# Performance work log

Measured on AMD Instinct MI355X. Metric: run time of the kernel, lower is better.

## Reference

```python
import jax, jax.numpy as jnp
import numpy as np
import math

D_MODEL = 1024
NUM_HEADS = 16
HEAD_DIM = D_MODEL // NUM_HEADS
GAMMA = 1.0
B, T = 2, 2048
PHI_F = 8


def setup_inputs() -> dict:
    key = jax.random.key(0)
    ks = jax.random.split(key, 16)
    s = 0.02
    return {
        "query": jax.random.normal(ks[0], (B, T, D_MODEL), jnp.float32),
        "key": jax.random.normal(ks[1], (B, T, D_MODEL), jnp.float32),
        "value": jax.random.normal(ks[2], (B, T, D_MODEL), jnp.float32),
        "phi": jax.random.uniform(ks[3], (B, T, PHI_F), jnp.float32),
        "logvar": jax.random.normal(ks[4], (B, T, PHI_F), jnp.float32),
        "Wq": jax.random.normal(ks[5], (D_MODEL, D_MODEL), jnp.float32) * s,
        "bq": jnp.zeros((D_MODEL,), jnp.float32),
        "Wk": jax.random.normal(ks[6], (D_MODEL, D_MODEL), jnp.float32) * s,
        "bk": jnp.zeros((D_MODEL,), jnp.float32),
        "Wv": jax.random.normal(ks[7], (D_MODEL, D_MODEL), jnp.float32) * s,
        "bv": jnp.zeros((D_MODEL,), jnp.float32),
        "Wo": jax.random.normal(ks[8], (D_MODEL, D_MODEL), jnp.float32) * s,
        "bo": jnp.zeros((D_MODEL,), jnp.float32),
        "w_sigma": jnp.float32(1.0),
        "w_phi": jnp.float32(1.0),
    }


def reference(query, key, value, phi, logvar, Wq, bq, Wk, bk, Wv, bv, Wo, bo, w_sigma, w_phi):
    Bsz, Tq, _ = query.shape
    # projections (torch Linear: x @ W.T + b), split into heads -> (B, H, T, hd)
    def proj(x, W, b):
        return (x @ W.T + b).reshape(Bsz, Tq, NUM_HEADS, HEAD_DIM).transpose(0, 2, 1, 3)
    q = proj(query, Wq, bq)
    k = proj(key, Wk, bk)
    v = proj(value, Wv, bv)
    # raw scores (B, H, Tq, Tk)
    scores = jnp.einsum("bhqd,bhkd->bhqk", q, k) / math.sqrt(HEAD_DIM)
    # per-query token scalar biases: mean over feature dim -> (B, 1, T, 1)
    lv = logvar.mean(axis=-1)[:, None, :, None]
    ph = phi.mean(axis=-1)[:, None, :, None]
    scores = scores - w_sigma * lv
    scores = (scores - w_phi * (1.0 - ph)) / jnp.maximum(ph ** GAMMA, 1e-6)
    attn = jax.nn.softmax(scores, axis=-1)
    out = jnp.einsum("bhqk,bhkd->bhqd", attn, v)
    out = out.transpose(0, 2, 1, 3).reshape(Bsz, Tq, D_MODEL)
    return out @ Wo.T + bo
```

## Files before the change

kernel.cpp:

```cpp
#include <hip/hip_runtime.h>


typedef __bf16 bf16x8 __attribute__((ext_vector_type(8)));
typedef __bf16 bf16x4 __attribute__((ext_vector_type(4)));
typedef float f32x4 __attribute__((ext_vector_type(4)));
typedef unsigned short u16;
typedef unsigned int u32;
typedef u16 u16x8 __attribute__((ext_vector_type(8)));

#define GLD_TO_LDS(g, l) __builtin_amdgcn_global_load_lds( \
    (const __attribute__((address_space(1))) void*)(g),    \
    (__attribute__((address_space(3))) void*)(l), 16, 0, 0)

__device__ __forceinline__ u16 f2b(float f) {
  u32 u = __builtin_bit_cast(u32, f);
  u += 0x7fffu + ((u >> 16) & 1u);
  return (u16)(u >> 16);
}

__global__ __launch_bounds__(256) void prep_kernel(
    const float* __restrict__ query, const float* __restrict__ key,
    const float* __restrict__ value, const float* __restrict__ Wq,
    const float* __restrict__ Wk, const float* __restrict__ Wv,
    const float* __restrict__ Wo, const float* __restrict__ phi,
    u16* __restrict__ Xq, u16* __restrict__ Xk, u16* __restrict__ Xv,
    u16* __restrict__ Wqb, u16* __restrict__ Wkb, u16* __restrict__ Wvb,
    u16* __restrict__ Wob, float* __restrict__ rscale)
{
  const long gid = (long)blockIdx.x * 256 + threadIdx.x;
  const long e = gid * 4;
  const float* src; u16* dst; long off;
  if (e < 4194304L)       { src = query; dst = Xq;  off = e; }
  else if (e < 8388608L)  { src = key;   dst = Xk;  off = e - 4194304L; }
  else if (e < 12582912L) { src = value; dst = Xv;  off = e - 8388608L; }
  else if (e < 13631488L) { src = Wq;    dst = Wqb; off = e - 12582912L; }
  else if (e < 14680064L) { src = Wk;    dst = Wkb; off = e - 13631488L; }
  else if (e < 15728640L) { src = Wv;    dst = Wvb; off = e - 14680064L; }
  else                    { src = Wo;    dst = Wob; off = e - 15728640L; }
  const float4 v = *(const float4*)(src + off);
  ushort4 o;
  o.x = f2b(v.x); o.y = f2b(v.y); o.z = f2b(v.z); o.w = f2b(v.w);
  *(ushort4*)(dst + off) = o;

  if (gid < 4096) {
    const float4 p0 = *(const float4*)(phi + gid * 8);
    const float4 p1 = *(const float4*)(phi + gid * 8 + 4);
    const float mean = (p0.x + p0.y + p0.z + p0.w + p1.x + p1.y + p1.z + p1.w) * 0.125f;
    rscale[gid] = 1.4426950408889634f / (8.0f * fmaxf(mean, 1e-6f));
  }
}

template<int MODE>
__device__ __forceinline__ void gemm_body(
    u16 (*As)[4096], u16 (*Bs)[4096], int m0, int n0,
    const u16* __restrict__ A, const u16* __restrict__ Bw,
    const float* __restrict__ bias, void* __restrict__ Cout)
{
  constexpr int K = 1024;
  const int t = threadIdx.x;
  const int lane = t & 63, w = t >> 6;
  const int g = lane >> 4, c = lane & 15;
  const int srow = t >> 2, skc = (t & 3) * 8;
  const u16* gA = A + (size_t)(m0 + srow) * K + skc;
  const u16* gB = Bw + (size_t)(n0 + srow) * K + skc;
  const int wm = (w >> 1) * 64, wn = (w & 1) * 64;

  f32x4 acc[4][4] = {};

#define STG(b_, k0_) do {                              \
    GLD_TO_LDS(gA + (k0_), &As[b_][w * 512]);          \
    GLD_TO_LDS(gA + 64 * K + (k0_), &As[b_][w * 512 + 2048]); \
    GLD_TO_LDS(gB + (k0_), &Bs[b_][w * 512]);          \
    GLD_TO_LDS(gB + 64 * K + (k0_), &Bs[b_][w * 512 + 2048]); \
  } while (0)

  STG(0, 0);
  for (int i = 0; i < 32; ++i) {
    const int buf = i & 1;
    if (i < 31) {
      STG(buf ^ 1, (i + 1) * 32);
      asm volatile("s_waitcnt vmcnt(4)" ::: "memory");
    } else {
      asm volatile("s_waitcnt vmcnt(0)" ::: "memory");
    }
    __builtin_amdgcn_s_barrier();
    bf16x8 af[4], bfr[4];
#pragma unroll
    for (int mi = 0; mi < 4; ++mi)
      af[mi] = *(const bf16x8*)(&As[buf][0] + (wm + mi * 16 + c) * 32 + g * 8);
#pragma unroll
    for (int ni = 0; ni < 4; ++ni)
      bfr[ni] = *(const bf16x8*)(&Bs[buf][0] + (wn + ni * 16 + c) * 32 + g * 8);
#pragma unroll
    for (int mi = 0; mi < 4; ++mi)
#pragma unroll
      for (int ni = 0; ni < 4; ++ni)
        acc[mi][ni] = __builtin_amdgcn_mfma_f32_16x16x32_bf16(
            af[mi], bfr[ni], acc[mi][ni], 0, 0, 0);
    __builtin_amdgcn_s_barrier();
  }
#undef STG

#pragma unroll
  for (int ni = 0; ni < 4; ++ni) {
    const int ncol = n0 + wn + ni * 16 + c;
    const float bv = bias[ncol];
#pragma unroll
    for (int mi = 0; mi < 4; ++mi) {
#pragma unroll
      for (int r = 0; r < 4; ++r) {
        const int mrow = m0 + wm + mi * 16 + g * 4 + r;
        const float val = acc[mi][ni][r] + bv;
        if (MODE == 0) {
          const int bb = mrow >> 11, tt = mrow & 2047;
          const int hh = ncol >> 6, dd = ncol & 63;
          ((u16*)Cout)[((((size_t)bb * 16 + hh) * 2048 + tt) << 6) + dd] = f2b(val);
        } else {
          ((float*)Cout)[(size_t)mrow * 1024 + ncol] = val;
        }
      }
    }
  }
}

__global__ __launch_bounds__(256) void gemm_qkv_kernel(
    const u16* __restrict__ Xq, const u16* __restrict__ Xk, const u16* __restrict__ Xv,
    const u16* __restrict__ Wqb, const u16* __restrict__ Wkb, const u16* __restrict__ Wvb,
    const float* __restrict__ bq, const float* __restrict__ bk, const float* __restrict__ bv,
    u16* __restrict__ Qh, u16* __restrict__ Kh, u16* __restrict__ Vh)
{
  __shared__ __align__(16) u16 As[2][4096], Bs[2][4096];
  const u32 n = blockIdx.z * 256u + blockIdx.y * 8u + blockIdx.x;
  const u32 nl = (n & 7u) * 96u + (n >> 3);
  const int bx = nl & 7, by = (nl >> 3) & 31, bz = nl >> 8;
  const u16* A = (bz == 0) ? Xq : (bz == 1) ? Xk : Xv;
  const u16* W = (bz == 0) ? Wqb : (bz == 1) ? Wkb : Wvb;
  const float* bias = (bz == 0) ? bq : (bz == 1) ? bk : bv;
  u16* C = (bz == 0) ? Qh : (bz == 1) ? Kh : Vh;
  gemm_body<0>(As, Bs, by * 128, bx * 128, A, W, bias, C);
}

__global__ __launch_bounds__(256) void gemm_o_kernel(
    const u16* __restrict__ Oh, const u16* __restrict__ Wob,
    const float* __restrict__ bo, float* __restrict__ out)
{
  __shared__ __align__(16) u16 As[2][4096], Bs[2][4096];
  const u32 n = blockIdx.y * 8u + blockIdx.x;
  const u32 nl = (n & 7u) * 32u + (n >> 3);
  gemm_body<1>(As, Bs, (int)(nl >> 3) * 128, (int)(nl & 7) * 128, Oh, Wob, bo, out);
}

__global__ __launch_bounds__(256) void transpose_v_kernel(
    const u16* __restrict__ Vh, u16* __restrict__ Vt)
{
  __shared__ __align__(16) u16 tile[64][72];
  const int bh = blockIdx.y, t0 = blockIdx.x * 64;
  const int tid = threadIdx.x;
  const int r = tid >> 3, cc = (tid & 7) * 8;
  const u16* src = Vh + ((size_t)bh * 2048 + t0) * 64;
#pragma unroll
  for (int it = 0; it < 2; ++it)
    *(u16x8*)&tile[r + 32 * it][cc] = *(const u16x8*)(src + (size_t)(r + 32 * it) * 64 + cc);
  __syncthreads();
  u16* dst = Vt + (size_t)bh * 64 * 2048 + t0;
#pragma unroll
  for (int it = 0; it < 2; ++it) {
    const int d = r + 32 * it;
    u16x8 v;
#pragma unroll
    for (int j = 0; j < 8; ++j) v[j] = tile[cc + j][d];
    *(u16x8*)(dst + (size_t)d * 2048 + cc) = v;
  }
}

__global__ __launch_bounds__(256) void attn_kernel(
    const u16* __restrict__ Qh, const u16* __restrict__ Kh,
    const u16* __restrict__ Vt, const float* __restrict__ rscale,
    u16* __restrict__ Oh)
{
  __shared__ __align__(16) u16 Ks[2][4096];
  __shared__ __align__(16) u16 Vs[2][4096];

  const u32 orig = blockIdx.y * 32 + blockIdx.x;
  const u32 newL = (orig & 7u) * 128u + (orig >> 3);
  const int qx = newL & 31, bh = newL >> 5;
  const int b = bh >> 4, h = bh & 15;

  const int t = threadIdx.x;
  const int w = t >> 6, lane = t & 63;
  const int g = lane >> 4, c = lane & 15;
  const int q0 = qx * 64 + w * 16;
  const int swz = (c & 7) << 4;

  const u16* Qb = Qh + (size_t)bh * (2048 * 64);
  const u16* Kb = Kh + (size_t)bh * (2048 * 64);
  const u16* Vb = Vt + (size_t)bh * (64 * 2048);

  const int sr = t >> 3;
  const int sx = ((t & 7) ^ (sr & 7)) * 8;

  const float rs = rscale[b * 2048 + q0 + c];
  bf16x8 qf0, qf1;
  {
    const u16x8 a0 = *(const u16x8*)(Qb + (size_t)(q0 + c) * 64 + g * 8);
    const u16x8 a1 = *(const u16x8*)(Qb + (size_t)(q0 + c) * 64 + 32 + g * 8);
    u16x8 o0, o1;
#pragma unroll
    for (int j = 0; j < 8; ++j) {
      o0[j] = f2b(__builtin_bit_cast(float, (u32)a0[j] << 16) * rs);
      o1[j] = f2b(__builtin_bit_cast(float, (u32)a1[j] << 16) * rs);
    }
    qf0 = __builtin_bit_cast(bf16x8, o0);
    qf1 = __builtin_bit_cast(bf16x8, o1);
  }

  float m = -3.0e38f, l = 0.0f;
  f32x4 acc[4] = {};

#define STAGE(buf_, kc_) do {                                         \
    const u16* kg0 = Kb + (size_t)((kc_) + sr) * 64 + sx;             \
    const u16* kg1 = Kb + (size_t)((kc_) + 32 + sr) * 64 + sx;        \
    const u16* vg0 = Vb + (size_t)sr * 2048 + (kc_) + sx;             \
    const u16* vg1 = Vb + (size_t)(32 + sr) * 2048 + (kc_) + sx;      \
    u16* kd = &Ks[buf_][w * 512];                                     \
    u16* vd = &Vs[buf_][w * 512];                                     \
    GLD_TO_LDS(kg0, kd);                                              \
    GLD_TO_LDS(kg1, kd + 2048);                                       \
    GLD_TO_LDS(vg0, vd);                                              \
    GLD_TO_LDS(vg1, vd + 2048);                                       \
  } while (0)

  STAGE(0, 0);

  for (int kc = 0; kc < 2048; kc += 64) {
    const int buf = (kc >> 6) & 1;
    if (kc + 64 < 2048) {
      STAGE(buf ^ 1, kc + 64);
      asm volatile("s_waitcnt vmcnt(4)" ::: "memory");
    } else {
      asm volatile("s_waitcnt vmcnt(0)" ::: "memory");
    }
    __builtin_amdgcn_s_barrier();

    const u16* Kt = &Ks[buf][0];
    const u16* Vq = &Vs[buf][0];

    f32x4 s[4];
#pragma unroll
    for (int j = 0; j < 4; ++j) {
      const int rk = j * 16 + c;
      const bf16x8 k0 = *(const bf16x8*)(Kt + rk * 64 + ((((g << 4)) ^ swz) >> 1));
      const bf16x8 k1 = *(const bf16x8*)(Kt + rk * 64 + (((64 | (g << 4)) ^ swz) >> 1));
      const f32x4 z = {};
      s[j] = __builtin_amdgcn_mfma_f32_16x16x32_bf16(k0, qf0, z, 0, 0, 0);
      s[j] = __builtin_amdgcn_mfma_f32_16x16x32_bf16(k1, qf1, s[j], 0, 0, 0);
    }

    float tl = s[0][0];
#pragma unroll
    for (int j = 0; j < 4; ++j)
#pragma unroll
      for (int r = 0; r < 4; ++r) tl = fmaxf(tl, s[j][r]);
    if (__any(tl > m + 8.0f)) {
      tl = fmaxf(tl, __shfl_xor(tl, 16));
      tl = fmaxf(tl, __shfl_xor(tl, 32));
      const float mn = fmaxf(m, tl);
      const float corr = __builtin_amdgcn_exp2f(m - mn);
      m = mn;
      l *= corr;
#pragma unroll
      for (int dt = 0; dt < 4; ++dt)
#pragma unroll
        for (int r = 0; r < 4; ++r) acc[dt][r] *= corr;
    }

    float p[4][4];
#pragma unroll
    for (int j = 0; j < 4; ++j)
#pragma unroll
      for (int r = 0; r < 4; ++r) {
        p[j][r] = __builtin_amdgcn_exp2f(s[j][r] - m);
        l += p[j][r];
      }
    bf16x8 pb0, pb1;
#pragma unroll
    for (int jj = 0; jj < 8; ++jj) {
      pb0[jj] = (__bf16)p[jj >> 2][jj & 3];
      pb1[jj] = (__bf16)p[2 + (jj >> 2)][jj & 3];
    }

#pragma unroll
    for (int dt = 0; dt < 4; ++dt) {
      const int rv = dt * 16 + c;
      const u16* vrow = Vq + rv * 64;
      const int xr = (rv & 7) << 4;
      bf16x8 va0, va1;
      const bf16x4 a0 = *(const bf16x4*)(vrow + (((g * 8) ^ xr) >> 1));
      const bf16x4 a1 = *(const bf16x4*)(vrow + (((32 + g * 8) ^ xr) >> 1));
      const bf16x4 a2 = *(const bf16x4*)(vrow + (((64 + g * 8) ^ xr) >> 1));
      const bf16x4 a3 = *(const bf16x4*)(vrow + (((96 + g * 8) ^ xr) >> 1));
#pragma unroll
      for (int j = 0; j < 4; ++j) {
        va0[j] = a0[j]; va0[4 + j] = a1[j];
        va1[j] = a2[j]; va1[4 + j] = a3[j];
      }
      acc[dt] = __builtin_amdgcn_mfma_f32_16x16x32_bf16(va0, pb0, acc[dt], 0, 0, 0);
      acc[dt] = __builtin_amdgcn_mfma_f32_16x16x32_bf16(va1, pb1, acc[dt], 0, 0, 0);
    }

    __builtin_amdgcn_s_barrier();
  }
#undef STAGE

  l += __shfl_xor(l, 16);
  l += __shfl_xor(l, 32);
  const float inv = 1.0f / l;

#pragma unroll
  for (int dt = 0; dt < 4; ++dt)
#pragma unroll
    for (int r = 0; r < 4; ++r) {
      const int trow = q0 + c;
      const int dd = dt * 16 + g * 4 + r;
      Oh[(((size_t)b * 2048 + trow) * 16 + h) * 64 + dd] = f2b(acc[dt][r] * inv);
    }
}

extern "C" void kernel_launch(void* const* d_in, const int* in_sizes, int n_in,
                              void* d_out, int out_size, void* d_ws, size_t ws_size,
                              hipStream_t stream) {
  const float* query = (const float*)d_in[0];
  const float* key_  = (const float*)d_in[1];
  const float* value = (const float*)d_in[2];
  const float* phi   = (const float*)d_in[3];
  const float* Wq = (const float*)d_in[5];
  const float* bq = (const float*)d_in[6];
  const float* Wk = (const float*)d_in[7];
  const float* bk = (const float*)d_in[8];
  const float* Wv = (const float*)d_in[9];
  const float* bv = (const float*)d_in[10];
  const float* Wo = (const float*)d_in[11];
  const float* bo = (const float*)d_in[12];

  char* ws = (char*)d_ws;
  const size_t MB = 1u << 20;
  u16* Xq  = (u16*)(ws);
  u16* Xk  = (u16*)(ws + 8 * MB);
  u16* Xv  = (u16*)(ws + 16 * MB);
  u16* Wqb = (u16*)(ws + 24 * MB);
  u16* Wkb = (u16*)(ws + 26 * MB);
  u16* Wvb = (u16*)(ws + 28 * MB);
  u16* Wob = (u16*)(ws + 30 * MB);
  u16* Qh  = (u16*)(ws + 32 * MB);
  u16* Kh  = (u16*)(ws + 40 * MB);
  u16* Vh  = (u16*)(ws + 48 * MB);
  float* rscale = (float*)(ws + 56 * MB);
  u16* Oh = Xq;
  u16* Vt = Xk;

  prep_kernel<<<16384, 256, 0, stream>>>(query, key_, value, Wq, Wk, Wv, Wo, phi,
                                         Xq, Xk, Xv, Wqb, Wkb, Wvb, Wob, rscale);
  gemm_qkv_kernel<<<dim3(8, 32, 3), 256, 0, stream>>>(Xq, Xk, Xv, Wqb, Wkb, Wvb,
                                                      bq, bk, bv, Qh, Kh, Vh);
  transpose_v_kernel<<<dim3(32, 32), 256, 0, stream>>>(Vh, Vt);
  attn_kernel<<<dim3(32, 32), 256, 0, stream>>>(Qh, Kh, Vt, rscale, Oh);
  gemm_o_kernel<<<dim3(8, 32), 256, 0, stream>>>(Oh, Wob, bo, (float*)d_out);
}
```

Baseline: 258.4 us.

## Fuse V transpose into QKV GEMM epilogue, shuffle P operand, add MFMA priority

The V projection epilogue now writes the transposed (d-major) layout directly, which removes the separate transpose kernel and its round trip through global memory. In the attention kernel, V fragments are read as full 16-byte swizzled LDS loads, and the P operand is redistributed across lanes with shuffles so that its layout matches. s_setprio is raised around MFMA clusters in both the GEMM and attention loops. The costs are strided 2-byte scattered stores in the V epilogue, extra cross-lane shuffles per iteration, and a dependence on the new lane mapping being correct.

```diff
diff --git a/kernel.cpp b/kernel.cpp
--- a/kernel.cpp
+++ b/kernel.cpp
@@ -2,11 +2,12 @@
 
 
 typedef __bf16 bf16x8 __attribute__((ext_vector_type(8)));
-typedef __bf16 bf16x4 __attribute__((ext_vector_type(4)));
+typedef __bf16 bf16x2 __attribute__((ext_vector_type(2)));
 typedef float f32x4 __attribute__((ext_vector_type(4)));
 typedef unsigned short u16;
 typedef unsigned int u32;
 typedef u16 u16x8 __attribute__((ext_vector_type(8)));
+typedef u32 u32x4 __attribute__((ext_vector_type(4)));
 
 #define GLD_TO_LDS(g, l) __builtin_amdgcn_global_load_lds( \
     (const __attribute__((address_space(1))) void*)(g),    \
@@ -91,12 +92,14 @@
 #pragma unroll
     for (int ni = 0; ni < 4; ++ni)
       bfr[ni] = *(const bf16x8*)(&Bs[buf][0] + (wn + ni * 16 + c) * 32 + g * 8);
+    __builtin_amdgcn_s_setprio(1);
 #pragma unroll
     for (int mi = 0; mi < 4; ++mi)
 #pragma unroll
       for (int ni = 0; ni < 4; ++ni)
         acc[mi][ni] = __builtin_amdgcn_mfma_f32_16x16x32_bf16(
             af[mi], bfr[ni], acc[mi][ni], 0, 0, 0);
+    __builtin_amdgcn_s_setprio(0);
     __builtin_amdgcn_s_barrier();
   }
 #undef STG
@@ -115,6 +118,10 @@
           const int bb = mrow >> 11, tt = mrow & 2047;
           const int hh = ncol >> 6, dd = ncol & 63;
           ((u16*)Cout)[((((size_t)bb * 16 + hh) * 2048 + tt) << 6) + dd] = f2b(val);
+        } else if (MODE == 2) {
+          const int bb = mrow >> 11, tt = mrow & 2047;
+          const int hh = ncol >> 6, dd = ncol & 63;
+          ((u16*)Cout)[((((size_t)bb * 16 + hh) * 64 + dd) << 11) + tt] = f2b(val);
         } else {
           ((float*)Cout)[(size_t)mrow * 1024 + ncol] = val;
         }
@@ -127,17 +134,19 @@
     const u16* __restrict__ Xq, const u16* __restrict__ Xk, const u16* __restrict__ Xv,
     const u16* __restrict__ Wqb, const u16* __restrict__ Wkb, const u16* __restrict__ Wvb,
     const float* __restrict__ bq, const float* __restrict__ bk, const float* __restrict__ bv,
-    u16* __restrict__ Qh, u16* __restrict__ Kh, u16* __restrict__ Vh)
+    u16* __restrict__ Qh, u16* __restrict__ Kh, u16* __restrict__ Vt)
 {
   __shared__ __align__(16) u16 As[2][4096], Bs[2][4096];
   const u32 n = blockIdx.z * 256u + blockIdx.y * 8u + blockIdx.x;
   const u32 nl = (n & 7u) * 96u + (n >> 3);
   const int bx = nl & 7, by = (nl >> 3) & 31, bz = nl >> 8;
-  const u16* A = (bz == 0) ? Xq : (bz == 1) ? Xk : Xv;
-  const u16* W = (bz == 0) ? Wqb : (bz == 1) ? Wkb : Wvb;
-  const float* bias = (bz == 0) ? bq : (bz == 1) ? bk : bv;
-  u16* C = (bz == 0) ? Qh : (bz == 1) ? Kh : Vh;
-  gemm_body<0>(As, Bs, by * 128, bx * 128, A, W, bias, C);
+  if (bz == 2) {
+    gemm_body<2>(As, Bs, by * 128, bx * 128, Xv, Wvb, bv, Vt);
+  } else if (bz == 1) {
+    gemm_body<0>(As, Bs, by * 128, bx * 128, Xk, Wkb, bk, Kh);
+  } else {
+    gemm_body<0>(As, Bs, by * 128, bx * 128, Xq, Wqb, bq, Qh);
+  }
 }
 
 __global__ __launch_bounds__(256) void gemm_o_kernel(
@@ -148,29 +157,6 @@
   const u32 n = blockIdx.y * 8u + blockIdx.x;
   const u32 nl = (n & 7u) * 32u + (n >> 3);
   gemm_body<1>(As, Bs, (int)(nl >> 3) * 128, (int)(nl & 7) * 128, Oh, Wob, bo, out);
-}
-
-__global__ __launch_bounds__(256) void transpose_v_kernel(
-    const u16* __restrict__ Vh, u16* __restrict__ Vt)
-{
-  __shared__ __align__(16) u16 tile[64][72];
-  const int bh = blockIdx.y, t0 = blockIdx.x * 64;
-  const int tid = threadIdx.x;
-  const int r = tid >> 3, cc = (tid & 7) * 8;
-  const u16* src = Vh + ((size_t)bh * 2048 + t0) * 64;
-#pragma unroll
-  for (int it = 0; it < 2; ++it)
-    *(u16x8*)&tile[r + 32 * it][cc] = *(const u16x8*)(src + (size_t)(r + 32 * it) * 64 + cc);
-  __syncthreads();
-  u16* dst = Vt + (size_t)bh * 64 * 2048 + t0;
-#pragma unroll
-  for (int it = 0; it < 2; ++it) {
-    const int d = r + 32 * it;
-    u16x8 v;
-#pragma unroll
-    for (int j = 0; j < 8; ++j) v[j] = tile[cc + j][d];
-    *(u16x8*)(dst + (size_t)d * 2048 + cc) = v;
-  }
 }
 
 __global__ __launch_bounds__(256) void attn_kernel(
@@ -216,6 +202,9 @@
 
   float m = -3.0e38f, l = 0.0f;
   f32x4 acc[4] = {};
+  const int src0 = ((g & 1) << 5) + c;
+  const int src1 = src0 + 16;
+  const bool hig = (g >> 1) != 0;
 
 #define STAGE(buf_, kc_) do {                                         \
     const u16* kg0 = Kb + (size_t)((kc_) + sr) * 64 + sx;             \
@@ -252,8 +241,19 @@
       const bf16x8 k0 = *(const bf16x8*)(Kt + rk * 64 + ((((g << 4)) ^ swz) >> 1));
       const bf16x8 k1 = *(const bf16x8*)(Kt + rk * 64 + (((64 | (g << 4)) ^ swz) >> 1));
       const f32x4 z = {};
+      __builtin_amdgcn_s_setprio(1);
       s[j] = __builtin_amdgcn_mfma_f32_16x16x32_bf16(k0, qf0, z, 0, 0, 0);
       s[j] = __builtin_amdgcn_mfma_f32_16x16x32_bf16(k1, qf1, s[j], 0, 0, 0);
+      __builtin_amdgcn_s_setprio(0);
+    }
+
+    bf16x8 vf[4][2];
+#pragma unroll
+    for (int dt = 0; dt < 4; ++dt) {
+      const int rv = dt * 16 + c;
+#pragma unroll
+      for (int kk = 0; kk < 2; ++kk)
+        vf[dt][kk] = *(const bf16x8*)(Vq + rv * 64 + ((((kk << 6) | (g << 4)) ^ swz) >> 1));
     }
 
     float tl = s[0][0];
@@ -282,31 +282,42 @@
         p[j][r] = __builtin_amdgcn_exp2f(s[j][r] - m);
         l += p[j][r];
       }
-    bf16x8 pb0, pb1;
-#pragma unroll
-    for (int jj = 0; jj < 8; ++jj) {
-      pb0[jj] = (__bf16)p[jj >> 2][jj & 3];
-      pb1[jj] = (__bf16)p[2 + (jj >> 2)][jj & 3];
-    }
-
+    u32 W[4][2];
+#pragma unroll
+    for (int j = 0; j < 4; ++j)
+#pragma unroll
+      for (int rp = 0; rp < 2; ++rp) {
+        bf16x2 t2;
+        t2[0] = (__bf16)p[j][2 * rp];
+        t2[1] = (__bf16)p[j][2 * rp + 1];
+        W[j][rp] = __builtin_bit_cast(u32, t2);
+      }
+    u32 R[4][2][2];
+#pragma unroll
+    for (int q = 0; q < 4; ++q)
+#pragma unroll
+      for (int rp = 0; rp < 2; ++rp) {
+        R[q][rp][0] = (u32)__shfl((int)W[q][rp], src0);
+        R[q][rp][1] = (u32)__shfl((int)W[q][rp], src1);
+      }
+    u32x4 pw0, pw1;
+#pragma unroll
+    for (int gs = 0; gs < 2; ++gs)
+#pragma unroll
+      for (int rp = 0; rp < 2; ++rp) {
+        pw0[gs * 2 + rp] = hig ? R[1][rp][gs] : R[0][rp][gs];
+        pw1[gs * 2 + rp] = hig ? R[3][rp][gs] : R[2][rp][gs];
+      }
+    const bf16x8 pb0 = __builtin_bit_cast(bf16x8, pw0);
+    const bf16x8 pb1 = __builtin_bit_cast(bf16x8, pw1);
+
+    __builtin_amdgcn_s_setprio(1);
 #pragma unroll
     for (int dt = 0; dt < 4; ++dt) {
-      const int rv = dt * 16 + c;
-      const u16* vrow = Vq + rv * 64;
-      const int xr = (rv & 7) << 4;
-      bf16x8 va0, va1;
-      const bf16x4 a0 = *(const bf16x4*)(vrow + (((g * 8) ^ xr) >> 1));
-      const bf16x4 a1 = *(const bf16x4*)(vrow + (((32 + g * 8) ^ xr) >> 1));
-      const bf16x4 a2 = *(const bf16x4*)(vrow + (((64 + g * 8) ^ xr) >> 1));
-      const bf16x4 a3 = *(const bf16x4*)(vrow + (((96 + g * 8) ^ xr) >> 1));
-#pragma unroll
-      for (int j = 0; j < 4; ++j) {
-        va0[j] = a0[j]; va0[4 + j] = a1[j];
-        va1[j] = a2[j]; va1[4 + j] = a3[j];
-      }
-      acc[dt] = __builtin_amdgcn_mfma_f32_16x16x32_bf16(va0, pb0, acc[dt], 0, 0, 0);
-      acc[dt] = __builtin_amdgcn_mfma_f32_16x16x32_bf16(va1, pb1, acc[dt], 0, 0, 0);
-    }
+      acc[dt] = __builtin_amdgcn_mfma_f32_16x16x32_bf16(vf[dt][0], pb0, acc[dt], 0, 0, 0);
+      acc[dt] = __builtin_amdgcn_mfma_f32_16x16x32_bf16(vf[dt][1], pb1, acc[dt], 0, 0, 0);
+    }
+    __builtin_amdgcn_s_setprio(0);
 
     __builtin_amdgcn_s_barrier();
   }
@@ -353,16 +364,14 @@
   u16* Wob = (u16*)(ws + 30 * MB);
   u16* Qh  = (u16*)(ws + 32 * MB);
   u16* Kh  = (u16*)(ws + 40 * MB);
-  u16* Vh  = (u16*)(ws + 48 * MB);
+  u16* Vt  = (u16*)(ws + 48 * MB);
   float* rscale = (float*)(ws + 56 * MB);
   u16* Oh = Xq;
-  u16* Vt = Xk;
 
   prep_kernel<<<16384, 256, 0, stream>>>(query, key_, value, Wq, Wk, Wv, Wo, phi,
                                          Xq, Xk, Xv, Wqb, Wkb, Wvb, Wob, rscale);
   gemm_qkv_kernel<<<dim3(8, 32, 3), 256, 0, stream>>>(Xq, Xk, Xv, Wqb, Wkb, Wvb,
-                                                      bq, bk, bv, Qh, Kh, Vh);
-  transpose_v_kernel<<<dim3(32, 32), 256, 0, stream>>>(Vh, Vt);
+                                                      bq, bk, bv, Qh, Kh, Vt);
   attn_kernel<<<dim3(32, 32), 256, 0, stream>>>(Qh, Kh, Vt, rscale, Oh);
   gemm_o_kernel<<<dim3(8, 32), 256, 0, stream>>>(Oh, Wob, bo, (float*)d_out);
 }
```

After: 296.9 us. 14.9% more time.

## Hoist V LDS reads before softmax, add setprio around MFMAs, extend V swizzle

Applied to the files above, without the earlier changes.

Moves the V fragment LDS reads ahead of the softmax so their latency overlaps the exp computations. It brackets MFMA groups with s_setprio so the scheduler favors matrix work across waves. It also adds an extra XOR bit to the V tile swizzle, matched in the transpose kernel, to reduce LDS bank conflicts. The cost is higher register pressure from holding the V fragments, and the swizzle must stay consistent between the writer and reader kernels.

```diff
diff --git a/kernel.cpp b/kernel.cpp
--- a/kernel.cpp
+++ b/kernel.cpp
@@ -163,12 +163,13 @@
     *(u16x8*)&tile[r + 32 * it][cc] = *(const u16x8*)(src + (size_t)(r + 32 * it) * 64 + cc);
   __syncthreads();
   u16* dst = Vt + (size_t)bh * 64 * 2048 + t0;
+  const int sw = (r & 8) ? 4 : 0;
 #pragma unroll
   for (int it = 0; it < 2; ++it) {
     const int d = r + 32 * it;
     u16x8 v;
 #pragma unroll
-    for (int j = 0; j < 8; ++j) v[j] = tile[cc + j][d];
+    for (int j = 0; j < 8; ++j) v[j] = tile[cc + (j ^ sw)][d];
     *(u16x8*)(dst + (size_t)d * 2048 + cc) = v;
   }
 }
@@ -252,8 +253,24 @@
       const bf16x8 k0 = *(const bf16x8*)(Kt + rk * 64 + ((((g << 4)) ^ swz) >> 1));
       const bf16x8 k1 = *(const bf16x8*)(Kt + rk * 64 + (((64 | (g << 4)) ^ swz) >> 1));
       const f32x4 z = {};
+      __builtin_amdgcn_s_setprio(1);
       s[j] = __builtin_amdgcn_mfma_f32_16x16x32_bf16(k0, qf0, z, 0, 0, 0);
       s[j] = __builtin_amdgcn_mfma_f32_16x16x32_bf16(k1, qf1, s[j], 0, 0, 0);
+      __builtin_amdgcn_s_setprio(0);
+    }
+
+    bf16x8 va[4][2];
+#pragma unroll
+    for (int dt = 0; dt < 4; ++dt) {
+      const int rv = dt * 16 + c;
+      const u16* vrow = Vq + rv * 64;
+      const int xr = ((rv & 7) << 4) | (rv & 8);
+      const bf16x4 a0 = *(const bf16x4*)(vrow + (((g * 8) ^ xr) >> 1));
+      const bf16x4 a1 = *(const bf16x4*)(vrow + (((32 + g * 8) ^ xr) >> 1));
+      const bf16x4 a2 = *(const bf16x4*)(vrow + (((64 + g * 8) ^ xr) >> 1));
+      const bf16x4 a3 = *(const bf16x4*)(vrow + (((96 + g * 8) ^ xr) >> 1));
+      va[dt][0] = __builtin_shufflevector(a0, a1, 0, 1, 2, 3, 4, 5, 6, 7);
+      va[dt][1] = __builtin_shufflevector(a2, a3, 0, 1, 2, 3, 4, 5, 6, 7);
     }
 
     float tl = s[0][0];
@@ -274,39 +291,32 @@
         for (int r = 0; r < 4; ++r) acc[dt][r] *= corr;
     }
 
-    float p[4][4];
+    f32x4 pv[4];
 #pragma unroll
     for (int j = 0; j < 4; ++j)
 #pragma unroll
-      for (int r = 0; r < 4; ++r) {
-        p[j][r] = __builtin_amdgcn_exp2f(s[j][r] - m);
-        l += p[j][r];
-      }
-    bf16x8 pb0, pb1;
-#pragma unroll
-    for (int jj = 0; jj < 8; ++jj) {
-      pb0[jj] = (__bf16)p[jj >> 2][jj & 3];
-      pb1[jj] = (__bf16)p[2 + (jj >> 2)][jj & 3];
-    }
-
+      for (int r = 0; r < 4; ++r) pv[j][r] = __builtin_amdgcn_exp2f(s[j][r] - m);
+#pragma unroll
+    for (int j = 0; j < 4; ++j)
+      l += pv[j][0] + pv[j][1] + pv[j][2] + pv[j][3];
+    bf16x4 pc[4];
+#pragma unroll
+    for (int j = 0; j < 4; ++j) {
+      pc[j][0] = (__bf16)pv[j][0];
+      pc[j][1] = (__bf16)pv[j][1];
+      pc[j][2] = (__bf16)pv[j][2];
+      pc[j][3] = (__bf16)pv[j][3];
+    }
+    const bf16x8 pb0 = __builtin_shufflevector(pc[0], pc[1], 0, 1, 2, 3, 4, 5, 6, 7);
+    const bf16x8 pb1 = __builtin_shufflevector(pc[2], pc[3], 0, 1, 2, 3, 4, 5, 6, 7);
+
+    __builtin_amdgcn_s_setprio(1);
 #pragma unroll
     for (int dt = 0; dt < 4; ++dt) {
-      const int rv = dt * 16 + c;
-      const u16* vrow = Vq + rv * 64;
-      const int xr = (rv & 7) << 4;
-      bf16x8 va0, va1;
-      const bf16x4 a0 = *(const bf16x4*)(vrow + (((g * 8) ^ xr) >> 1));
-      const bf16x4 a1 = *(const bf16x4*)(vrow + (((32 + g * 8) ^ xr) >> 1));
-      const bf16x4 a2 = *(const bf16x4*)(vrow + (((64 + g * 8) ^ xr) >> 1));
-      const bf16x4 a3 = *(const bf16x4*)(vrow + (((96 + g * 8) ^ xr) >> 1));
-#pragma unroll
-      for (int j = 0; j < 4; ++j) {
-        va0[j] = a0[j]; va0[4 + j] = a1[j];
-        va1[j] = a2[j]; va1[4 + j] = a3[j];
-      }
-      acc[dt] = __builtin_amdgcn_mfma_f32_16x16x32_bf16(va0, pb0, acc[dt], 0, 0, 0);
-      acc[dt] = __builtin_amdgcn_mfma_f32_16x16x32_bf16(va1, pb1, acc[dt], 0, 0, 0);
-    }
+      acc[dt] = __builtin_amdgcn_mfma_f32_16x16x32_bf16(va[dt][0], pb0, acc[dt], 0, 0, 0);
+      acc[dt] = __builtin_amdgcn_mfma_f32_16x16x32_bf16(va[dt][1], pb1, acc[dt], 0, 0, 0);
+    }
+    __builtin_amdgcn_s_setprio(0);
 
     __builtin_amdgcn_s_barrier();
   }
```

Result: no change. 257.9 us (-0.2%).
